# Optimization experiments

Hardware: AMD Instinct MI355X
Metric: run time of the kernel (lower is better)

## Reference

```python
import jax, jax.numpy as jnp
import numpy as np

N = 50000
E = 100000
D = 768


def setup_inputs() -> dict:
    key = jax.random.key(0)
    ks = jax.random.split(key, 8)
    x = jax.random.normal(ks[0], (N, D), dtype=jnp.float32)
    edge_index = jax.random.randint(ks[1], (2, E), 0, N, dtype=jnp.int64)
    s = 1.0 / np.sqrt(D)
    W1l = jax.random.uniform(ks[2], (D, D), jnp.float32, -s, s)
    b1l = jax.random.uniform(ks[3], (D,), jnp.float32, -s, s)
    W1r = jax.random.uniform(ks[4], (D, D), jnp.float32, -s, s)
    W2l = jax.random.uniform(ks[5], (D, D), jnp.float32, -s, s)
    b2l = jax.random.uniform(ks[6], (D,), jnp.float32, -s, s)
    W2r = jax.random.uniform(ks[7], (D, D), jnp.float32, -s, s)
    return {"x": x, "edge_index": edge_index, "W1l": W1l, "b1l": b1l,
            "W1r": W1r, "W2l": W2l, "b2l": b2l, "W2r": W2r}


def sage_conv(x, src, dst, Wl, bl, Wr):
    # mean-aggregate neighbor (source) features at target nodes
    summed = jax.ops.segment_sum(x[src], dst, num_segments=N)  # [N, D]
    deg = jax.ops.segment_sum(jnp.ones((src.shape[0],), x.dtype), dst,
                              num_segments=N)
    agg = summed / jnp.clip(deg, 1.0)[:, None]
    # lin_l(agg) + lin_r(x)  (PyG SAGEConv: lin_l has bias, lin_r does not)
    return agg @ Wl.T + bl + x @ Wr.T


def reference(x, edge_index, W1l, b1l, W1r, W2l, b2l, W2r):
    src, dst = edge_index[0], edge_index[1]
    h = sage_conv(x, src, dst, W1l, b1l, W1r)
    h = jax.nn.relu(h)
    return sage_conv(h, src, dst, W2l, b2l, W2r)
```

## Files before the change

### kernel.cpp

```cpp
#include <hip/hip_runtime.h>
#include <stdint.h>

#define NN 50000
#define NE 100000
#define DD 768
#define KC 1536
#define SCAN_B 196
#define BM 128
#define BN 256
#define BK 64
#define NTM 391
#define NTN 3

typedef __attribute__((ext_vector_type(8))) __bf16 bf16x8;
typedef __attribute__((ext_vector_type(4))) float floatx4;

static __device__ __forceinline__ float bf2f(unsigned short u) {
    union { unsigned int u; float f; } c; c.u = ((unsigned int)u) << 16; return c.f;
}
static __device__ __forceinline__ unsigned short f2bf(float f) {
    union { float f; unsigned int u; } c; c.f = f;
    return (unsigned short)((c.u + 0x7FFFu + ((c.u >> 16) & 1u)) >> 16);
}

static __device__ __forceinline__ void gld16(const void* g, void* l) {
    __builtin_amdgcn_global_load_lds(
        (const __attribute__((address_space(1))) unsigned int*)g,
        (__attribute__((address_space(3))) unsigned int*)l, 16, 0, 0);
}


__global__ __launch_bounds__(192) void k_convert_x(const float* __restrict__ x,
                                                   unsigned short* __restrict__ acat) {
    const int n = blockIdx.x;
    const int c = threadIdx.x * 4;
    const float4 v = *(const float4*)(x + (size_t)n * DD + c);
    ushort4 o;
    o.x = f2bf(v.x); o.y = f2bf(v.y); o.z = f2bf(v.z); o.w = f2bf(v.w);
    *(ushort4*)(acat + (size_t)n * KC + DD + c) = o;
}

__global__ __launch_bounds__(384) void k_convert_w(const float* __restrict__ W1l,
                                                   const float* __restrict__ W1r,
                                                   const float* __restrict__ W2l,
                                                   const float* __restrict__ W2r,
                                                   unsigned short* __restrict__ B1,
                                                   unsigned short* __restrict__ B2) {
    const int j = blockIdx.x;
    const int layer = blockIdx.y;
    const int k = threadIdx.x * 4;
    const float* Wl = layer ? W2l : W1l;
    const float* Wr = layer ? W2r : W1r;
    unsigned short* B = layer ? B2 : B1;
    const float4 v = (k < DD) ? *(const float4*)(Wl + (size_t)j * DD + k)
                              : *(const float4*)(Wr + (size_t)j * DD + (k - DD));
    ushort4 o; o.x = f2bf(v.x); o.y = f2bf(v.y); o.z = f2bf(v.z); o.w = f2bf(v.w);
    *(ushort4*)(B + (size_t)j * KC + k) = o;
}


__global__ __launch_bounds__(256) void k_hist(const int* __restrict__ dst,
                                              int* __restrict__ cnt) {
    int e = blockIdx.x * 256 + threadIdx.x;
    if (e < NE) atomicAdd(&cnt[dst[e]], 1);
}

__global__ __launch_bounds__(256) void k_scan1(const int* __restrict__ cnt,
                                               int* __restrict__ rowptr,
                                               int* __restrict__ partial) {
    __shared__ int buf[256];
    const int t = threadIdx.x;
    const int i = blockIdx.x * 256 + t;
    int v = (i < NN) ? cnt[i] : 0;
    buf[t] = v;
    __syncthreads();
#pragma unroll
    for (int off = 1; off < 256; off <<= 1) {
        int u = (t >= off) ? buf[t - off] : 0;
        __syncthreads();
        buf[t] += u;
        __syncthreads();
    }
    if (i < NN) rowptr[i + 1] = buf[t];
    if (t == 255) partial[blockIdx.x] = buf[255];
}

__global__ __launch_bounds__(256) void k_scan2(int* __restrict__ partial) {
    __shared__ int buf[256];
    const int t = threadIdx.x;
    int v = (t < SCAN_B) ? partial[t] : 0;
    buf[t] = v;
    __syncthreads();
#pragma unroll
    for (int off = 1; off < 256; off <<= 1) {
        int u = (t >= off) ? buf[t - off] : 0;
        __syncthreads();
        buf[t] += u;
        __syncthreads();
    }
    if (t < SCAN_B) partial[t] = buf[t] - v;
}

__global__ __launch_bounds__(256) void k_scan3(int* __restrict__ rowptr,
                                               const int* __restrict__ partial) {
    const int i = blockIdx.x * 256 + threadIdx.x;
    if (i < NN) rowptr[i + 1] += partial[blockIdx.x];
    if (i == 0) rowptr[0] = 0;
}

__global__ __launch_bounds__(256) void k_fill(const int* __restrict__ src,
                                              const int* __restrict__ dst,
                                              const int* __restrict__ rowptr,
                                              int* __restrict__ cursor,
                                              int* __restrict__ esrc) {
    int e = blockIdx.x * 256 + threadIdx.x;
    if (e < NE) {
        const int d = dst[e];
        const int pos = atomicAdd(&cursor[d], 1);
        esrc[rowptr[d] + pos] = src[e];
    }
}

__global__ __launch_bounds__(192) void k_agg(const unsigned short* __restrict__ srcmat,
                                             const int* __restrict__ rowptr,
                                             const int* __restrict__ esrc,
                                             unsigned short* __restrict__ dstmat) {
    const int n = blockIdx.x;
    const int c = threadIdx.x * 4;
    const int beg = rowptr[n], end = rowptr[n + 1];
    float4 a = {0.f, 0.f, 0.f, 0.f};
    for (int e = beg; e < end; ++e) {
        const int s = esrc[e];
        const ushort4 v = *(const ushort4*)(srcmat + (size_t)s * KC + DD + c);
        a.x += bf2f(v.x); a.y += bf2f(v.y); a.z += bf2f(v.z); a.w += bf2f(v.w);
    }
    const float inv = (end > beg) ? 1.0f / (float)(end - beg) : 1.0f;
    ushort4 o;
    o.x = f2bf(a.x * inv); o.y = f2bf(a.y * inv);
    o.z = f2bf(a.z * inv); o.w = f2bf(a.w * inv);
    *(ushort4*)(dstmat + (size_t)n * KC + c) = o;
}

template <int MODE>
__global__ __launch_bounds__(512) void k_gemm(const unsigned short* __restrict__ A,
                                              const unsigned short* __restrict__ B,
                                              const float* __restrict__ bias,
                                              unsigned short* __restrict__ outA,
                                              float* __restrict__ outF) {
    __shared__ alignas(16) unsigned short sA[3][BM * BK];
    __shared__ alignas(16) unsigned short sB[3][BN * BK];
    const int tid = threadIdx.x;
    const int w = tid >> 6, lane = tid & 63;
    const int quad = lane >> 4, r16 = lane & 15;
    const int wr = w >> 2, wc = w & 3;
    const int wm = wr * 64, wn = wc * 64;

    const int nwg = NTM * NTN;
    const int q = nwg >> 3, r = nwg & 7;
    const int xcd = blockIdx.x & 7, slot = blockIdx.x >> 3;
    const int L = (xcd < r ? xcd * (q + 1) : r * (q + 1) + (xcd - r) * q) + slot;
    const int tn = L % NTN;
    const int tm = L / NTN;
    const int rowBase = tm * BM;

    floatx4 acc[4][4];
#pragma unroll
    for (int i = 0; i < 4; ++i)
#pragma unroll
        for (int j = 0; j < 4; ++j) acc[i][j] = (floatx4){0.f, 0.f, 0.f, 0.f};

    const unsigned short* aS[2];
    const unsigned short* bS[4];
#pragma unroll
    for (int l = 0; l < 2; ++l) {
        const int c = l * 512 + tid;
        const int row = c >> 3;
        const int jd = ((c & 7) ^ (row & 7)) * 8;
        int gr = rowBase + row; if (gr > NN - 1) gr = NN - 1;
        aS[l] = A + (size_t)gr * KC + jd;
    }
#pragma unroll
    for (int l = 0; l < 4; ++l) {
        const int c = l * 512 + tid;
        const int row = c >> 3;
        const int jd = ((c & 7) ^ (row & 7)) * 8;
        bS[l] = B + (size_t)(tn * BN + row) * KC + jd;
    }

    auto stageK = [&](int d, int half) {
        if (half == 0) {
            gld16(aS[0], &sA[d][(0 * 512 + w * 64) * 8]);
            gld16(aS[1], &sA[d][(1 * 512 + w * 64) * 8]);
            gld16(bS[0], &sB[d][(0 * 512 + w * 64) * 8]);
        } else {
            gld16(bS[1], &sB[d][(1 * 512 + w * 64) * 8]);
            gld16(bS[2], &sB[d][(2 * 512 + w * 64) * 8]);
            gld16(bS[3], &sB[d][(3 * 512 + w * 64) * 8]);
            aS[0] += BK; aS[1] += BK;
            bS[0] += BK; bS[1] += BK; bS[2] += BK; bS[3] += BK;
        }
    };

    auto phase = [&](int s, int p, int d, int doStage) {
        const int physc = ((p * 4 + quad) ^ (r16 & 7)) * 8;
        bf16x8 af[4], bfr[4];
#pragma unroll
        for (int mf = 0; mf < 4; ++mf)
            af[mf] = *(const bf16x8*)(&sA[s][(wm + mf * 16 + r16) * BK + physc]);
#pragma unroll
        for (int nf = 0; nf < 4; ++nf)
            bfr[nf] = *(const bf16x8*)(&sB[s][(wn + nf * 16 + r16) * BK + physc]);
        if (doStage) stageK(d, p);
        __builtin_amdgcn_sched_barrier(0);
        __builtin_amdgcn_s_barrier();
        __builtin_amdgcn_sched_barrier(0);
        __builtin_amdgcn_s_setprio(1);
#pragma unroll
        for (int mf = 0; mf < 4; ++mf)
#pragma unroll
            for (int nf = 0; nf < 4; ++nf)
                acc[mf][nf] = __builtin_amdgcn_mfma_f32_16x16x32_bf16(af[mf], bfr[nf], acc[mf][nf], 0, 0, 0);
        __builtin_amdgcn_s_setprio(0);
        __builtin_amdgcn_sched_barrier(0);
    };

#define SB                                            \
    do {                                              \
        __builtin_amdgcn_s_barrier();                 \
        __builtin_amdgcn_sched_barrier(0);            \
    } while (0)
#define VW(N)                                             \
    do {                                                  \
        __builtin_amdgcn_sched_barrier(0);                \
        asm volatile("s_waitcnt vmcnt(" #N ")" ::: "memory"); \
    } while (0)

    stageK(0, 0); stageK(0, 1);
    stageK(1, 0); stageK(1, 1);
    VW(6);
    SB;

#pragma unroll 1
    for (int g = 0; g < 7; ++g) {
        phase(0, 0, 2, 1); SB; phase(0, 1, 2, 1); VW(6); SB;
        phase(1, 0, 0, 1); SB; phase(1, 1, 0, 1); VW(6); SB;
        phase(2, 0, 1, 1); SB; phase(2, 1, 1, 1); VW(6); SB;
    }
    phase(0, 0, 2, 1); SB; phase(0, 1, 2, 1); VW(6); SB;
    phase(1, 0, 0, 0); SB; phase(1, 1, 0, 0); VW(0); SB;
    phase(2, 0, 0, 0); SB; phase(2, 1, 0, 0);
#undef SB
#undef VW

#pragma unroll
    for (int mf = 0; mf < 4; ++mf)
#pragma unroll
        for (int nf = 0; nf < 4; ++nf) {
            const int gcol = tn * BN + wn + nf * 16 + r16;
            const float bv = bias[gcol];
#pragma unroll
            for (int rr = 0; rr < 4; ++rr) {
                const int grow = rowBase + wm + mf * 16 + quad * 4 + rr;
                if (grow < NN) {
                    float v = acc[mf][nf][rr] + bv;
                    if (MODE == 0) {
                        v = fmaxf(v, 0.0f);
                        outA[(size_t)grow * KC + DD + gcol] = f2bf(v);
                    } else {
                        outF[(size_t)grow * DD + gcol] = v;
                    }
                }
            }
        }
}

extern "C" void kernel_launch(void* const* d_in, const int* in_sizes, int n_in,
                              void* d_out, int out_size, void* d_ws, size_t ws_size,
                              hipStream_t stream) {
    const float* x   = (const float*)d_in[0];
    const int*   ei  = (const int*)d_in[1];
    const float* W1l = (const float*)d_in[2];
    const float* b1l = (const float*)d_in[3];
    const float* W1r = (const float*)d_in[4];
    const float* W2l = (const float*)d_in[5];
    const float* b2l = (const float*)d_in[6];
    const float* W2r = (const float*)d_in[7];
    const int* src = ei;
    const int* dst = ei + NE;
    float* out = (float*)d_out;

    char* ws = (char*)d_ws;
    unsigned short* Acat1 = (unsigned short*)ws;
    unsigned short* Acat2 = (unsigned short*)(ws + (size_t)NN * KC * 2);
    unsigned short* B1    = (unsigned short*)(ws + (size_t)NN * KC * 4);
    unsigned short* B2    = B1 + (size_t)DD * KC;
    int* cnt    = (int*)(ws + (size_t)NN * KC * 4 + (size_t)DD * KC * 4);
    int* rowptr = cnt + NN;
    int* esrc   = rowptr + NN + 1;
    int* partial = esrc + NE;

    hipMemsetAsync(cnt, 0, NN * sizeof(int), stream);
    k_hist<<<(NE + 255) / 256, 256, 0, stream>>>(dst, cnt);
    k_scan1<<<SCAN_B, 256, 0, stream>>>(cnt, rowptr, partial);
    k_scan2<<<1, 256, 0, stream>>>(partial);
    k_scan3<<<SCAN_B, 256, 0, stream>>>(rowptr, partial);
    hipMemsetAsync(cnt, 0, NN * sizeof(int), stream);
    k_fill<<<(NE + 255) / 256, 256, 0, stream>>>(src, dst, rowptr, cnt, esrc);

    k_convert_x<<<NN, 192, 0, stream>>>(x, Acat1);
    dim3 wgrid(DD, 2);
    k_convert_w<<<wgrid, 384, 0, stream>>>(W1l, W1r, W2l, W2r, B1, B2);

    const int ggrid = NTM * NTN;

    k_agg<<<NN, 192, 0, stream>>>(Acat1, rowptr, esrc, Acat1);
    k_gemm<0><<<ggrid, 512, 0, stream>>>(Acat1, B1, b1l, Acat2, nullptr);

    k_agg<<<NN, 192, 0, stream>>>(Acat2, rowptr, esrc, Acat2);
    k_gemm<1><<<ggrid, 512, 0, stream>>>(Acat2, B2, b2l, nullptr, out);
}
```

Baseline: 727.3 us.

## Merge GEMM half-phases into one barrier-separated segment per K tile

The triple-buffered bf16 MFMA main loop now handles a whole BK=64 tile per segment instead of two half-tile phases. Each segment reads both k-halves of the fragments from LDS, issues all six global-to-LDS loads for the next stage at once, then runs 32 MFMAs. There is now a single wait-plus-barrier per tile instead of several barriers and sched_barriers. This cuts synchronisation and scheduling fences in the hot loop, at the cost of more live fragment registers and less interleaving between loads and MFMAs.

New measurement: 705.5 us. 1.03x faster.

```diff
diff --git a/kernel.cpp b/kernel.cpp
--- a/kernel.cpp
+++ b/kernel.cpp
@@ -187,70 +187,67 @@
         bS[l] = B + (size_t)(tn * BN + row) * KC + jd;
     }
 
-    auto stageK = [&](int d, int half) {
-        if (half == 0) {
-            gld16(aS[0], &sA[d][(0 * 512 + w * 64) * 8]);
-            gld16(aS[1], &sA[d][(1 * 512 + w * 64) * 8]);
-            gld16(bS[0], &sB[d][(0 * 512 + w * 64) * 8]);
-        } else {
-            gld16(bS[1], &sB[d][(1 * 512 + w * 64) * 8]);
-            gld16(bS[2], &sB[d][(2 * 512 + w * 64) * 8]);
-            gld16(bS[3], &sB[d][(3 * 512 + w * 64) * 8]);
-            aS[0] += BK; aS[1] += BK;
-            bS[0] += BK; bS[1] += BK; bS[2] += BK; bS[3] += BK;
-        }
+    auto stageK = [&](int d) {
+        gld16(aS[0], &sA[d][(0 * 512 + w * 64) * 8]);
+        gld16(aS[1], &sA[d][(1 * 512 + w * 64) * 8]);
+        gld16(bS[0], &sB[d][(0 * 512 + w * 64) * 8]);
+        gld16(bS[1], &sB[d][(1 * 512 + w * 64) * 8]);
+        gld16(bS[2], &sB[d][(2 * 512 + w * 64) * 8]);
+        gld16(bS[3], &sB[d][(3 * 512 + w * 64) * 8]);
+        aS[0] += BK; aS[1] += BK;
+        bS[0] += BK; bS[1] += BK; bS[2] += BK; bS[3] += BK;
     };
 
-    auto phase = [&](int s, int p, int d, int doStage) {
-        const int physc = ((p * 4 + quad) ^ (r16 & 7)) * 8;
-        bf16x8 af[4], bfr[4];
+    const int pc0 = ((0 * 4 + quad) ^ (r16 & 7)) * 8;
+    const int pc1 = ((1 * 4 + quad) ^ (r16 & 7)) * 8;
+
+    auto seg = [&](int s, int d, int doStage) {
+        bf16x8 a0[4], b0[4], a1[4], b1[4];
 #pragma unroll
         for (int mf = 0; mf < 4; ++mf)
-            af[mf] = *(const bf16x8*)(&sA[s][(wm + mf * 16 + r16) * BK + physc]);
+            a0[mf] = *(const bf16x8*)(&sA[s][(wm + mf * 16 + r16) * BK + pc0]);
 #pragma unroll
         for (int nf = 0; nf < 4; ++nf)
-            bfr[nf] = *(const bf16x8*)(&sB[s][(wn + nf * 16 + r16) * BK + physc]);
-        if (doStage) stageK(d, p);
-        __builtin_amdgcn_sched_barrier(0);
-        __builtin_amdgcn_s_barrier();
-        __builtin_amdgcn_sched_barrier(0);
+            b0[nf] = *(const bf16x8*)(&sB[s][(wn + nf * 16 + r16) * BK + pc0]);
+#pragma unroll
+        for (int mf = 0; mf < 4; ++mf)
+            a1[mf] = *(const bf16x8*)(&sA[s][(wm + mf * 16 + r16) * BK + pc1]);
+#pragma unroll
+        for (int nf = 0; nf < 4; ++nf)
+            b1[nf] = *(const bf16x8*)(&sB[s][(wn + nf * 16 + r16) * BK + pc1]);
+        if (doStage) stageK(d);
         __builtin_amdgcn_s_setprio(1);
 #pragma unroll
         for (int mf = 0; mf < 4; ++mf)
 #pragma unroll
             for (int nf = 0; nf < 4; ++nf)
-                acc[mf][nf] = __builtin_amdgcn_mfma_f32_16x16x32_bf16(af[mf], bfr[nf], acc[mf][nf], 0, 0, 0);
+                acc[mf][nf] = __builtin_amdgcn_mfma_f32_16x16x32_bf16(a0[mf], b0[nf], acc[mf][nf], 0, 0, 0);
+#pragma unroll
+        for (int mf = 0; mf < 4; ++mf)
+#pragma unroll
+            for (int nf = 0; nf < 4; ++nf)
+                acc[mf][nf] = __builtin_amdgcn_mfma_f32_16x16x32_bf16(a1[mf], b1[nf], acc[mf][nf], 0, 0, 0);
         __builtin_amdgcn_s_setprio(0);
-        __builtin_amdgcn_sched_barrier(0);
     };
 
-#define SB                                            \
-    do {                                              \
-        __builtin_amdgcn_s_barrier();                 \
-        __builtin_amdgcn_sched_barrier(0);            \
-    } while (0)
-#define VW(N)                                             \
+#define BND(N)                                            \
     do {                                                  \
         __builtin_amdgcn_sched_barrier(0);                \
         asm volatile("s_waitcnt vmcnt(" #N ")" ::: "memory"); \
+        __builtin_amdgcn_s_barrier();                     \
     } while (0)
 
-    stageK(0, 0); stageK(0, 1);
-    stageK(1, 0); stageK(1, 1);
-    VW(6);
-    SB;
-
+    stageK(0); stageK(1);
 #pragma unroll 1
     for (int g = 0; g < 7; ++g) {
-        phase(0, 0, 2, 1); SB; phase(0, 1, 2, 1); VW(6); SB;
-        phase(1, 0, 0, 1); SB; phase(1, 1, 0, 1); VW(6); SB;
-        phase(2, 0, 1, 1); SB; phase(2, 1, 1, 1); VW(6); SB;
-    }
-    phase(0, 0, 2, 1); SB; phase(0, 1, 2, 1); VW(6); SB;
-    phase(1, 0, 0, 0); SB; phase(1, 1, 0, 0); VW(0); SB;
-    phase(2, 0, 0, 0); SB; phase(2, 1, 0, 0);
-#undef SB
-#undef VW
+        BND(6); seg(0, 2, 1);
+        BND(6); seg(1, 0, 1);
+        BND(6); seg(2, 1, 1);
+    }
+    BND(6); seg(0, 2, 1);
+    BND(6); seg(1, 0, 0);
+    BND(0); seg(2, 0, 0);
+#undef BND
 
 #pragma unroll
     for (int mf = 0; mf < 4; ++mf)
```
